# Kernel optimization log

Measured on AMD Instinct MI355X. Metric: run time of the kernel, lower is better.

The kernel has to match this reference:

```python
import jax, jax.numpy as jnp
import numpy as np

DIM = 256
K = 16
EPS = 1e-5
B, N = 8, 2048


def setup_inputs() -> dict:
    key = jax.random.key(0)
    ks = jax.random.split(key, 24)
    D = DIM
    w = lambda i, shape: jax.random.normal(ks[i], shape, dtype=jnp.float32) * 0.05
    inp = {
        "x": jax.random.normal(ks[0], (B, N, D), dtype=jnp.float32) * 0.1,
        "pos": jax.random.normal(ks[1], (B, N, 3), dtype=jnp.float32),
        # to_q / to_k / to_v (torch Linear, no bias): weight (out, in)
        "Wq": w(2, (D, D)),
        "Wk": w(3, (D, D)),
        "Wv": w(4, (D, D)),
        # pos_mlp: Conv2d(3->D,1x1,no bias), BN(D), ReLU, Conv2d(D->D,1x1,no bias)
        "pm_w1": w(5, (D, 3)),
        "pm_g1": jnp.ones((D,), jnp.float32),
        "pm_b1": w(6, (D,)),
        "pm_m1": w(7, (D,)),
        "pm_v1": jax.random.uniform(ks[8], (D,), jnp.float32) + 0.5,
        "pm_w2": w(9, (D, D)),
        # attn_mlp: Conv2d(D->D), BN(D), ReLU, Conv2d(D->D)
        "am_w1": w(10, (D, D)),
        "am_g1": jnp.ones((D,), jnp.float32),
        "am_b1": w(11, (D,)),
        "am_m1": w(12, (D,)),
        "am_v1": jax.random.uniform(ks[13], (D,), jnp.float32) + 0.5,
        "am_w2": w(14, (D, D)),
        # final_linear (with bias)
        "Wf": w(15, (D, D)),
        "bf": w(16, (D,)),
    }
    return inp


def _bn(h, g, b, m, v):
    # eval-mode BatchNorm over channel (last) dim
    return (h - m) * jax.lax.rsqrt(v + EPS) * g + b


def reference(x, pos, Wq, Wk, Wv, pm_w1, pm_g1, pm_b1, pm_m1, pm_v1, pm_w2,
              am_w1, am_g1, am_b1, am_m1, am_v1, am_w2, Wf, bf):
    D = x.shape[-1]
    # kNN over squared euclidean distance (self included, as in kNN_torch)
    sq = jnp.sum(pos * pos, axis=-1)                       # (B,N)
    dist = sq[:, :, None] + sq[:, None, :] - 2.0 * jnp.einsum('bnc,bmc->bnm', pos, pos)
    knn_idx = jax.lax.top_k(-dist, K)[1]                   # (B,N,K)

    gather = jax.vmap(lambda f, i: f[i])                   # batched index_points
    knn_xyz = gather(pos, knn_idx)                         # (B,N,K,3)

    q = jnp.einsum('bnd,ed->bne', x, Wq)                   # (B,N,D)
    k = gather(jnp.einsum('bnd,ed->bne', x, Wk), knn_idx)  # (B,N,K,D)
    v = gather(jnp.einsum('bnd,ed->bne', x, Wv), knn_idx)  # (B,N,K,D)

    rel = pos[:, :, None] - knn_xyz                        # (B,N,K,3)
    pe = jnp.einsum('bnkc,dc->bnkd', rel, pm_w1)
    pe = jax.nn.relu(_bn(pe, pm_g1, pm_b1, pm_m1, pm_v1))
    pe = jnp.einsum('bnkc,dc->bnkd', pe, pm_w2)            # (B,N,K,D)

    a = q[:, :, None] - k + pe                             # (B,N,K,D)
    a = jnp.einsum('bnkc,dc->bnkd', a, am_w1)
    a = jax.nn.relu(_bn(a, am_g1, am_b1, am_m1, am_v1))
    a = jnp.einsum('bnkc,dc->bnkd', a, am_w2)

    attn = jax.nn.softmax(a / np.sqrt(D).astype(np.float32), axis=-2)  # softmax over K
    agg = jnp.sum(attn * (v + pe), axis=2)                 # (B,N,D)
    return jnp.einsum('bnd,ed->bne', agg, Wf) + bf + x
```

## Files before the change

### kernel.cpp

```cpp
#include <hip/hip_runtime.h>
#include <math.h>

#define DIM   256
#define KNN   16
#define NPTS  2048
#define NB    8
#define TOTPTS (NB * NPTS)
#define RSB   528

typedef __attribute__((ext_vector_type(8))) short bf16x8;
typedef __attribute__((ext_vector_type(4))) float f32x4;

__device__ __forceinline__ unsigned short f2b(float f) {
    unsigned u = __builtin_bit_cast(unsigned, f);
    return (unsigned short)((u + 0x7fffu + ((u >> 16) & 1u)) >> 16);
}
__device__ __forceinline__ unsigned pack2(float a, float b) {
    return (unsigned)f2b(a) | ((unsigned)f2b(b) << 16);
}

#define OFF_KNN 0u
#define OFF_Q   (1u << 20)
#define OFF_K   ((1u << 20) + (16u << 20))
#define OFF_V   ((1u << 20) + (32u << 20))
#define OFF_WB  (49u << 20)
#define OFF_PAR (OFF_WB + 7u * 65536u * 2u)

__global__ void prep_kernel(const float* __restrict__ Wq, const float* __restrict__ Wk,
                            const float* __restrict__ Wv, const float* __restrict__ pm_w2,
                            const float* __restrict__ am_w1, const float* __restrict__ am_w2,
                            const float* __restrict__ Wf,
                            const float* __restrict__ pm_g1, const float* __restrict__ pm_b1,
                            const float* __restrict__ pm_m1, const float* __restrict__ pm_v1,
                            const float* __restrict__ am_g1, const float* __restrict__ am_b1,
                            const float* __restrict__ am_m1, const float* __restrict__ am_v1,
                            unsigned short* __restrict__ wb,
                            float* __restrict__ pm_sc, float* __restrict__ pm_bo,
                            float* __restrict__ am_sc, float* __restrict__ am_bo) {
    const int tid = blockIdx.x * 256 + threadIdx.x;
    const float* srcs[7] = {Wq, Wk, Wv, pm_w2, am_w1, am_w2, Wf};
    for (int i = tid; i < 7 * 65536; i += gridDim.x * 256) {
        const int m = i >> 16, o = i & 65535;
        wb[i] = f2b(srcs[m][o]);
    }
    if (tid < 256) {
        float s = pm_g1[tid] * rsqrtf(pm_v1[tid] + 1e-5f);
        pm_sc[tid] = s;
        pm_bo[tid] = pm_b1[tid] - pm_m1[tid] * s;
        s = am_g1[tid] * rsqrtf(am_v1[tid] + 1e-5f);
        am_sc[tid] = s;
        am_bo[tid] = am_b1[tid] - am_m1[tid] * s;
    }
}

__global__ __launch_bounds__(256, 4)
void knn_kernel(const float* __restrict__ pos, int* __restrict__ knn_out) {
    const int pt = blockIdx.x;
    const int b  = pt >> 11;
    const int n  = pt & (NPTS - 1);
    const int t  = threadIdx.x;
    const float* __restrict__ posb = pos + (size_t)b * NPTS * 3;

    const float qx = posb[n * 3 + 0], qy = posb[n * 3 + 1], qz = posb[n * 3 + 2];
    const float sqn = __fadd_rn(__fadd_rn(__fmul_rn(qx, qx), __fmul_rn(qy, qy)),
                                __fmul_rn(qz, qz));
    float d[8];
    #pragma unroll
    for (int i = 0; i < 8; ++i) {
        const int m = t + (i << 8);
        const float mx = posb[m * 3 + 0], my = posb[m * 3 + 1], mz = posb[m * 3 + 2];
        const float sqm = __fadd_rn(__fadd_rn(__fmul_rn(mx, mx), __fmul_rn(my, my)),
                                    __fmul_rn(mz, mz));
        const float dot = __fadd_rn(__fadd_rn(__fmul_rn(qx, mx), __fmul_rn(qy, my)),
                                    __fmul_rn(qz, mz));
        d[i] = __fsub_rn(__fadd_rn(sqn, sqm), __fmul_rn(2.0f, dot));
    }

    __shared__ float sd[4];
    __shared__ int   sm[4];
    __shared__ int   swin;
    unsigned mask = 0;

    for (int r = 0; r < KNN; ++r) {
        float bd = 1e30f;
        int   bm = 0x7fffffff;
        #pragma unroll
        for (int i = 0; i < 8; ++i) {
            if (!((mask >> i) & 1u)) {
                const int m = t + (i << 8);
                if (d[i] < bd || (d[i] == bd && m < bm)) { bd = d[i]; bm = m; }
            }
        }
        #pragma unroll
        for (int off = 32; off >= 1; off >>= 1) {
            const float od = __shfl_xor(bd, off);
            const int   om = __shfl_xor(bm, off);
            if (od < bd || (od == bd && om < bm)) { bd = od; bm = om; }
        }
        const int w = t >> 6;
        if ((t & 63) == 0) { sd[w] = bd; sm[w] = bm; }
        __syncthreads();
        if (t == 0) {
            float fd = sd[0]; int fm = sm[0];
            #pragma unroll
            for (int w2 = 1; w2 < 4; ++w2)
                if (sd[w2] < fd || (sd[w2] == fd && sm[w2] < fm)) { fd = sd[w2]; fm = sm[w2]; }
            swin = fm;
            knn_out[(size_t)pt * KNN + r] = fm;
        }
        __syncthreads();
        const int win = swin;
        if ((win & 255) == t) mask |= 1u << (win >> 8);
        __syncthreads();
    }
}

__device__ __forceinline__ void mfma_stage(const unsigned char* __restrict__ act,
                                           const unsigned short* __restrict__ Wb,
                                           int qr, int sub, int cbase,
                                           f32x4 acc[4][4]) {
    #pragma unroll
    for (int kk = 0; kk < 8; ++kk) {
        const int kb = kk * 64 + sub * 16;
        bf16x8 afr[4], bfr[4];
        #pragma unroll
        for (int rt = 0; rt < 4; ++rt)
            afr[rt] = *(const bf16x8*)(act + (rt * 16 + qr) * RSB + kb);
        #pragma unroll
        for (int ct = 0; ct < 4; ++ct)
            bfr[ct] = *(const bf16x8*)(Wb + (size_t)(cbase + ct * 16 + qr) * DIM + kk * 32 + sub * 8);
        #pragma unroll
        for (int rt = 0; rt < 4; ++rt)
            #pragma unroll
            for (int ct = 0; ct < 4; ++ct)
                acc[rt][ct] = __builtin_amdgcn_mfma_f32_16x16x32_bf16(afr[rt], bfr[ct],
                                                                      acc[rt][ct], 0, 0, 0);
    }
}

__global__ __launch_bounds__(256, 2)
void qkv_mfma(const float* __restrict__ X, const unsigned short* __restrict__ wb,
              float* __restrict__ Q, float* __restrict__ Kf, float* __restrict__ Vf) {
    __shared__ uint4 act4[64 * RSB / 16];
    unsigned char* act = (unsigned char*)act4;
    const int t = threadIdx.x, lane = t & 63, w = t >> 6;
    const int qr = lane & 15, sub = lane >> 4;
    const int m0 = blockIdx.x * 64;
    const int mat = blockIdx.y;
    const unsigned short* __restrict__ Wb = wb + (size_t)mat * 65536;
    float* __restrict__ O = (mat == 0) ? Q : (mat == 1) ? Kf : Vf;

    {
        const int r = t >> 2;
        const float* __restrict__ src = X + (size_t)(m0 + r) * DIM;
        #pragma unroll
        for (int j = 0; j < 8; ++j) {
            const int col = (t & 3) * 8 + j * 32;
            const float4 f0 = *(const float4*)(src + col);
            const float4 f1 = *(const float4*)(src + col + 4);
            uint4 u;
            u.x = pack2(f0.x, f0.y); u.y = pack2(f0.z, f0.w);
            u.z = pack2(f1.x, f1.y); u.w = pack2(f1.z, f1.w);
            *(uint4*)(act + r * RSB + col * 2) = u;
        }
    }
    __syncthreads();

    f32x4 acc[4][4];
    #pragma unroll
    for (int rt = 0; rt < 4; ++rt)
        #pragma unroll
        for (int ct = 0; ct < 4; ++ct) acc[rt][ct] = (f32x4)(0.0f);

    mfma_stage(act, Wb, qr, sub, w * 64, acc);

    #pragma unroll
    for (int rt = 0; rt < 4; ++rt)
        #pragma unroll
        for (int ct = 0; ct < 4; ++ct) {
            const int c = w * 64 + ct * 16 + qr;
            #pragma unroll
            for (int reg = 0; reg < 4; ++reg)
                O[(size_t)(m0 + rt * 16 + sub * 4 + reg) * DIM + c] = acc[rt][ct][reg];
        }
}

__global__ __launch_bounds__(256, 2)
void fused_attn(const float* __restrict__ x, const float* __restrict__ pos,
                const int* __restrict__ knn,
                const float* __restrict__ qf, const float* __restrict__ kf,
                const float* __restrict__ vf,
                const unsigned short* __restrict__ wb,
                const float* __restrict__ pm_w1,
                const float* __restrict__ pm_sc, const float* __restrict__ pm_bo,
                const float* __restrict__ am_sc, const float* __restrict__ am_bo,
                const float* __restrict__ bfin,
                float* __restrict__ out) {
    __shared__ uint4 act4[64 * RSB / 16];
    __shared__ int   nb_lds[64];
    __shared__ float4 rel_lds[64];
    unsigned char* act = (unsigned char*)act4;

    const int t = threadIdx.x, lane = t & 63, w = t >> 6;
    const int qr = lane & 15, sub = lane >> 4;
    const int pt_base = blockIdx.x << 2;
    const int bbase = pt_base & ~(NPTS - 1);
    const int cbase = w * 64;

    if (t < 64) {
        const int pi = t >> 4;
        const int j = knn[(size_t)(pt_base + pi) * KNN + (t & 15)];
        nb_lds[t] = j;
        const float* __restrict__ pp = pos + (size_t)(pt_base + pi) * 3;
        const float* __restrict__ pj = pos + (size_t)(bbase + j) * 3;
        rel_lds[t] = make_float4(pp[0] - pj[0], pp[1] - pj[1], pp[2] - pj[2], 0.0f);
    }
    __syncthreads();

    {
        const int c = t;
        const float w0 = pm_w1[c * 3 + 0], w1 = pm_w1[c * 3 + 1], w2 = pm_w1[c * 3 + 2];
        const float sc = pm_sc[c], bo = pm_bo[c];
        for (int r = 0; r < 64; ++r) {
            const float4 rl = rel_lds[r];
            float h = fmaf(rl.z, w2, fmaf(rl.y, w1, rl.x * w0));
            h = fmaxf(fmaf(h, sc, bo), 0.0f);
            *(unsigned short*)(act + r * RSB + c * 2) = f2b(h);
        }
    }
    __syncthreads();

    f32x4 peacc[4][4];
    #pragma unroll
    for (int rt = 0; rt < 4; ++rt)
        #pragma unroll
        for (int ct = 0; ct < 4; ++ct) peacc[rt][ct] = (f32x4)(0.0f);
    mfma_stage(act, wb + 3u * 65536u, qr, sub, cbase, peacc);
    __syncthreads();

    int nbr[4][4];
    #pragma unroll
    for (int rt = 0; rt < 4; ++rt)
        #pragma unroll
        for (int reg = 0; reg < 4; ++reg)
            nbr[rt][reg] = nb_lds[rt * 16 + sub * 4 + reg];

    #pragma unroll
    for (int rt = 0; rt < 4; ++rt)
        #pragma unroll
        for (int ct = 0; ct < 4; ++ct) {
            const int c = cbase + ct * 16 + qr;
            const float qv = qf[(size_t)(pt_base + rt) * DIM + c];
            #pragma unroll
            for (int reg = 0; reg < 4; ++reg) {
                const float kv = kf[(size_t)(bbase + nbr[rt][reg]) * DIM + c];
                const float a0 = qv - kv + peacc[rt][ct][reg];
                *(unsigned short*)(act + (rt * 16 + sub * 4 + reg) * RSB + c * 2) = f2b(a0);
            }
        }
    __syncthreads();

    f32x4 acc2[4][4];
    #pragma unroll
    for (int rt = 0; rt < 4; ++rt)
        #pragma unroll
        for (int ct = 0; ct < 4; ++ct) acc2[rt][ct] = (f32x4)(0.0f);
    mfma_stage(act, wb + 4u * 65536u, qr, sub, cbase, acc2);
    __syncthreads();
    #pragma unroll
    for (int ct = 0; ct < 4; ++ct) {
        const int c = cbase + ct * 16 + qr;
        const float sc = am_sc[c], bo = am_bo[c];
        #pragma unroll
        for (int rt = 0; rt < 4; ++rt)
            #pragma unroll
            for (int reg = 0; reg < 4; ++reg) {
                const float h = fmaxf(fmaf(acc2[rt][ct][reg], sc, bo), 0.0f);
                *(unsigned short*)(act + (rt * 16 + sub * 4 + reg) * RSB + c * 2) = f2b(h);
            }
    }
    __syncthreads();

    #pragma unroll
    for (int rt = 0; rt < 4; ++rt)
        #pragma unroll
        for (int ct = 0; ct < 4; ++ct) acc2[rt][ct] = (f32x4)(0.0f);
    mfma_stage(act, wb + 5u * 65536u, qr, sub, cbase, acc2);

    #pragma unroll
    for (int rt = 0; rt < 4; ++rt)
        #pragma unroll
        for (int ct = 0; ct < 4; ++ct) {
            float m = -1e30f;
            #pragma unroll
            for (int reg = 0; reg < 4; ++reg) {
                acc2[rt][ct][reg] *= 0.0625f;
                m = fmaxf(m, acc2[rt][ct][reg]);
            }
            m = fmaxf(m, __shfl_xor(m, 16));
            m = fmaxf(m, __shfl_xor(m, 32));
            float s = 0.0f;
            #pragma unroll
            for (int reg = 0; reg < 4; ++reg) {
                const float e = __expf(acc2[rt][ct][reg] - m);
                acc2[rt][ct][reg] = e;
                s += e;
            }
            s += __shfl_xor(s, 16);
            s += __shfl_xor(s, 32);
            const float inv = 1.0f / s;
            #pragma unroll
            for (int reg = 0; reg < 4; ++reg) acc2[rt][ct][reg] *= inv;
        }

    float agg[4][4];
    #pragma unroll
    for (int rt = 0; rt < 4; ++rt)
        #pragma unroll
        for (int ct = 0; ct < 4; ++ct) {
            const int c = cbase + ct * 16 + qr;
            float p = 0.0f;
            #pragma unroll
            for (int reg = 0; reg < 4; ++reg) {
                const float vv = vf[(size_t)(bbase + nbr[rt][reg]) * DIM + c];
                p = fmaf(acc2[rt][ct][reg], vv + peacc[rt][ct][reg], p);
            }
            p += __shfl_xor(p, 16);
            p += __shfl_xor(p, 32);
            agg[rt][ct] = p;
        }
    __syncthreads();

    {
        unsigned* actw = (unsigned*)act;
        for (int i = t; i < 12 * RSB / 4; i += 256) actw[RSB + i] = 0;
        if (sub == 0) {
            #pragma unroll
            for (int rt = 0; rt < 4; ++rt)
                #pragma unroll
                for (int ct = 0; ct < 4; ++ct) {
                    const int c = cbase + ct * 16 + qr;
                    *(unsigned short*)(act + rt * RSB + c * 2) = f2b(agg[rt][ct]);
                }
        }
    }
    __syncthreads();

    f32x4 facc[4];
    #pragma unroll
    for (int ct = 0; ct < 4; ++ct) facc[ct] = (f32x4)(0.0f);
    const unsigned short* __restrict__ Wfb = wb + 6u * 65536u;
    #pragma unroll
    for (int kk = 0; kk < 8; ++kk) {
        const int kb = kk * 64 + sub * 16;
        const bf16x8 af = *(const bf16x8*)(act + qr * RSB + kb);
        #pragma unroll
        for (int ct = 0; ct < 4; ++ct) {
            const bf16x8 bfr = *(const bf16x8*)(Wfb + (size_t)(cbase + ct * 16 + qr) * DIM + kk * 32 + sub * 8);
            facc[ct] = __builtin_amdgcn_mfma_f32_16x16x32_bf16(af, bfr, facc[ct], 0, 0, 0);
        }
    }
    if (sub == 0) {
        #pragma unroll
        for (int ct = 0; ct < 4; ++ct) {
            const int c = cbase + ct * 16 + qr;
            #pragma unroll
            for (int reg = 0; reg < 4; ++reg) {
                const size_t row = (size_t)(pt_base + reg) * DIM + c;
                out[row] = facc[ct][reg] + bfin[c] + x[row];
            }
        }
    }
}

extern "C" void kernel_launch(void* const* d_in, const int* in_sizes, int n_in,
                              void* d_out, int out_size, void* d_ws, size_t ws_size,
                              hipStream_t stream) {
    const float* x     = (const float*)d_in[0];
    const float* pos   = (const float*)d_in[1];
    const float* Wq    = (const float*)d_in[2];
    const float* Wk    = (const float*)d_in[3];
    const float* Wv    = (const float*)d_in[4];
    const float* pm_w1 = (const float*)d_in[5];
    const float* pm_g1 = (const float*)d_in[6];
    const float* pm_b1 = (const float*)d_in[7];
    const float* pm_m1 = (const float*)d_in[8];
    const float* pm_v1 = (const float*)d_in[9];
    const float* pm_w2 = (const float*)d_in[10];
    const float* am_w1 = (const float*)d_in[11];
    const float* am_g1 = (const float*)d_in[12];
    const float* am_b1 = (const float*)d_in[13];
    const float* am_m1 = (const float*)d_in[14];
    const float* am_v1 = (const float*)d_in[15];
    const float* am_w2 = (const float*)d_in[16];
    const float* Wf    = (const float*)d_in[17];
    const float* bfin  = (const float*)d_in[18];
    float* out = (float*)d_out;

    char* ws = (char*)d_ws;
    int*            knn_idx = (int*)(ws + OFF_KNN);
    float*          qf = (float*)(ws + OFF_Q);
    float*          kf = (float*)(ws + OFF_K);
    float*          vf = (float*)(ws + OFF_V);
    unsigned short* wb = (unsigned short*)(ws + OFF_WB);
    float*          pm_sc = (float*)(ws + OFF_PAR);
    float*          pm_bo = pm_sc + 256;
    float*          am_sc = pm_sc + 512;
    float*          am_bo = pm_sc + 768;

    prep_kernel<<<448, 256, 0, stream>>>(Wq, Wk, Wv, pm_w2, am_w1, am_w2, Wf,
                                         pm_g1, pm_b1, pm_m1, pm_v1,
                                         am_g1, am_b1, am_m1, am_v1,
                                         wb, pm_sc, pm_bo, am_sc, am_bo);
    knn_kernel<<<TOTPTS, 256, 0, stream>>>(pos, knn_idx);
    qkv_mfma<<<dim3(TOTPTS / 64, 3), 256, 0, stream>>>(x, wb, qf, kf, vf);
    fused_attn<<<TOTPTS / 4, 256, 0, stream>>>(x, pos, knn_idx, qf, kf, vf, wb,
                                               pm_w1, pm_sc, pm_bo, am_sc, am_bo,
                                               bfin, out);
}
```

Measured before the change: 685.5 us.

## Use one wavefront per query in kNN and split fused attention over 8 waves

The kNN kernel now assigns one 64-lane wavefront per query point, so each lane holds 32 distances. The top-16 selection becomes wave-local shuffle reductions in which only the lane that owned the winner rescans its values, which removes the three block barriers per round and the shared-memory reduction. The fused attention kernel moves to 512 threads, with each wave covering 32 output columns instead of 64, which halves per-wave accumulator registers and adds waves to hide latency. The cost is more registers per kNN lane (32 distances) and more waves competing for barriers in the attention block.

```diff
diff --git a/kernel.cpp b/kernel.cpp
--- a/kernel.cpp
+++ b/kernel.cpp
@@ -53,21 +53,21 @@
     }
 }
 
-__global__ __launch_bounds__(256, 4)
+__global__ __launch_bounds__(256, 8)
 void knn_kernel(const float* __restrict__ pos, int* __restrict__ knn_out) {
-    const int pt = blockIdx.x;
-    const int b  = pt >> 11;
-    const int n  = pt & (NPTS - 1);
-    const int t  = threadIdx.x;
+    const int wid  = (blockIdx.x << 2) | (threadIdx.x >> 6);
+    const int lane = threadIdx.x & 63;
+    const int b = wid >> 11;
+    const int n = wid & (NPTS - 1);
     const float* __restrict__ posb = pos + (size_t)b * NPTS * 3;
 
     const float qx = posb[n * 3 + 0], qy = posb[n * 3 + 1], qz = posb[n * 3 + 2];
     const float sqn = __fadd_rn(__fadd_rn(__fmul_rn(qx, qx), __fmul_rn(qy, qy)),
                                 __fmul_rn(qz, qz));
-    float d[8];
-    #pragma unroll
-    for (int i = 0; i < 8; ++i) {
-        const int m = t + (i << 8);
+    float d[32];
+    #pragma unroll
+    for (int i = 0; i < 32; ++i) {
+        const int m = lane + (i << 6);
         const float mx = posb[m * 3 + 0], my = posb[m * 3 + 1], mz = posb[m * 3 + 2];
         const float sqm = __fadd_rn(__fadd_rn(__fmul_rn(mx, mx), __fmul_rn(my, my)),
                                     __fmul_rn(mz, mz));
@@ -76,42 +76,60 @@
         d[i] = __fsub_rn(__fadd_rn(sqn, sqm), __fmul_rn(2.0f, dot));
     }
 
-    __shared__ float sd[4];
-    __shared__ int   sm[4];
-    __shared__ int   swin;
-    unsigned mask = 0;
-
+    unsigned claimed = 0;
+    float bd = d[0];
+    int   bm = lane;
+    #pragma unroll
+    for (int i = 1; i < 32; ++i) {
+        const int m = lane + (i << 6);
+        if (d[i] < bd || (d[i] == bd && m < bm)) { bd = d[i]; bm = m; }
+    }
+
+    int keep = 0;
     for (int r = 0; r < KNN; ++r) {
-        float bd = 1e30f;
-        int   bm = 0x7fffffff;
-        #pragma unroll
-        for (int i = 0; i < 8; ++i) {
-            if (!((mask >> i) & 1u)) {
-                const int m = t + (i << 8);
-                if (d[i] < bd || (d[i] == bd && m < bm)) { bd = d[i]; bm = m; }
-            }
-        }
+        float wd = bd;
+        int   wm = bm;
         #pragma unroll
         for (int off = 32; off >= 1; off >>= 1) {
-            const float od = __shfl_xor(bd, off);
-            const int   om = __shfl_xor(bm, off);
-            if (od < bd || (od == bd && om < bm)) { bd = od; bm = om; }
-        }
-        const int w = t >> 6;
-        if ((t & 63) == 0) { sd[w] = bd; sm[w] = bm; }
-        __syncthreads();
-        if (t == 0) {
-            float fd = sd[0]; int fm = sm[0];
-            #pragma unroll
-            for (int w2 = 1; w2 < 4; ++w2)
-                if (sd[w2] < fd || (sd[w2] == fd && sm[w2] < fm)) { fd = sd[w2]; fm = sm[w2]; }
-            swin = fm;
-            knn_out[(size_t)pt * KNN + r] = fm;
-        }
-        __syncthreads();
-        const int win = swin;
-        if ((win & 255) == t) mask |= 1u << (win >> 8);
-        __syncthreads();
+            const float od = __shfl_xor(wd, off);
+            const int   om = __shfl_xor(wm, off);
+            if (od < wd || (od == wd && om < wm)) { wd = od; wm = om; }
+        }
+        if (lane == r) keep = wm;
+        if ((wm & 63) == lane) {
+            claimed |= 1u << (wm >> 6);
+            bd = 1e30f; bm = 0x7fffffff;
+            #pragma unroll
+            for (int i = 0; i < 32; ++i) {
+                if (!((claimed >> i) & 1u)) {
+                    const int m = lane + (i << 6);
+                    if (d[i] < bd || (d[i] == bd && m < bm)) { bd = d[i]; bm = m; }
+                }
+            }
+        }
+    }
+    if (lane < KNN) knn_out[(size_t)wid * KNN + lane] = keep;
+}
+
+__device__ __forceinline__ void mfma_stage2(const unsigned char* __restrict__ act,
+                                            const unsigned short* __restrict__ Wb,
+                                            int qr, int sub, int cbase,
+                                            f32x4 acc[4][2]) {
+    #pragma unroll
+    for (int kk = 0; kk < 8; ++kk) {
+        const int kb = kk * 64 + sub * 16;
+        bf16x8 afr[4];
+        #pragma unroll
+        for (int rt = 0; rt < 4; ++rt)
+            afr[rt] = *(const bf16x8*)(act + (rt * 16 + qr) * RSB + kb);
+        #pragma unroll
+        for (int ct = 0; ct < 2; ++ct) {
+            const bf16x8 bfr = *(const bf16x8*)(Wb + (size_t)(cbase + ct * 16 + qr) * DIM + kk * 32 + sub * 8);
+            #pragma unroll
+            for (int rt = 0; rt < 4; ++rt)
+                acc[rt][ct] = __builtin_amdgcn_mfma_f32_16x16x32_bf16(afr[rt], bfr,
+                                                                      acc[rt][ct], 0, 0, 0);
+        }
     }
 }
 
@@ -185,7 +203,7 @@
         }
 }
 
-__global__ __launch_bounds__(256, 2)
+__global__ __launch_bounds__(512, 4)
 void fused_attn(const float* __restrict__ x, const float* __restrict__ pos,
                 const int* __restrict__ knn,
                 const float* __restrict__ qf, const float* __restrict__ kf,
@@ -205,7 +223,7 @@
     const int qr = lane & 15, sub = lane >> 4;
     const int pt_base = blockIdx.x << 2;
     const int bbase = pt_base & ~(NPTS - 1);
-    const int cbase = w * 64;
+    const int cbase = w * 32;
 
     if (t < 64) {
         const int pi = t >> 4;
@@ -218,10 +236,13 @@
     __syncthreads();
 
     {
-        const int c = t;
+        const int c  = t & 255;
+        const int rh = t >> 8;
         const float w0 = pm_w1[c * 3 + 0], w1 = pm_w1[c * 3 + 1], w2 = pm_w1[c * 3 + 2];
         const float sc = pm_sc[c], bo = pm_bo[c];
-        for (int r = 0; r < 64; ++r) {
+        #pragma unroll
+        for (int rr = 0; rr < 32; ++rr) {
+            const int r = rh * 32 + rr;
             const float4 rl = rel_lds[r];
             float h = fmaf(rl.z, w2, fmaf(rl.y, w1, rl.x * w0));
             h = fmaxf(fmaf(h, sc, bo), 0.0f);
@@ -230,12 +251,12 @@
     }
     __syncthreads();
 
-    f32x4 peacc[4][4];
-    #pragma unroll
-    for (int rt = 0; rt < 4; ++rt)
-        #pragma unroll
-        for (int ct = 0; ct < 4; ++ct) peacc[rt][ct] = (f32x4)(0.0f);
-    mfma_stage(act, wb + 3u * 65536u, qr, sub, cbase, peacc);
+    f32x4 peacc[4][2];
+    #pragma unroll
+    for (int rt = 0; rt < 4; ++rt)
+        #pragma unroll
+        for (int ct = 0; ct < 2; ++ct) peacc[rt][ct] = (f32x4)(0.0f);
+    mfma_stage2(act, wb + 3u * 65536u, qr, sub, cbase, peacc);
     __syncthreads();
 
     int nbr[4][4];
@@ -248,7 +269,7 @@
     #pragma unroll
     for (int rt = 0; rt < 4; ++rt)
         #pragma unroll
-        for (int ct = 0; ct < 4; ++ct) {
+        for (int ct = 0; ct < 2; ++ct) {
             const int c = cbase + ct * 16 + qr;
             const float qv = qf[(size_t)(pt_base + rt) * DIM + c];
             #pragma unroll
@@ -260,15 +281,15 @@
         }
     __syncthreads();
 
-    f32x4 acc2[4][4];
-    #pragma unroll
-    for (int rt = 0; rt < 4; ++rt)
-        #pragma unroll
-        for (int ct = 0; ct < 4; ++ct) acc2[rt][ct] = (f32x4)(0.0f);
-    mfma_stage(act, wb + 4u * 65536u, qr, sub, cbase, acc2);
-    __syncthreads();
-    #pragma unroll
-    for (int ct = 0; ct < 4; ++ct) {
+    f32x4 acc2[4][2];
+    #pragma unroll
+    for (int rt = 0; rt < 4; ++rt)
+        #pragma unroll
+        for (int ct = 0; ct < 2; ++ct) acc2[rt][ct] = (f32x4)(0.0f);
+    mfma_stage2(act, wb + 4u * 65536u, qr, sub, cbase, acc2);
+    __syncthreads();
+    #pragma unroll
+    for (int ct = 0; ct < 2; ++ct) {
         const int c = cbase + ct * 16 + qr;
         const float sc = am_sc[c], bo = am_bo[c];
         #pragma unroll
@@ -284,13 +305,13 @@
     #pragma unroll
     for (int rt = 0; rt < 4; ++rt)
         #pragma unroll
-        for (int ct = 0; ct < 4; ++ct) acc2[rt][ct] = (f32x4)(0.0f);
-    mfma_stage(act, wb + 5u * 65536u, qr, sub, cbase, acc2);
-
-    #pragma unroll
-    for (int rt = 0; rt < 4; ++rt)
-        #pragma unroll
-        for (int ct = 0; ct < 4; ++ct) {
+        for (int ct = 0; ct < 2; ++ct) acc2[rt][ct] = (f32x4)(0.0f);
+    mfma_stage2(act, wb + 5u * 65536u, qr, sub, cbase, acc2);
+
+    #pragma unroll
+    for (int rt = 0; rt < 4; ++rt)
+        #pragma unroll
+        for (int ct = 0; ct < 2; ++ct) {
             float m = -1e30f;
             #pragma unroll
             for (int reg = 0; reg < 4; ++reg) {
@@ -313,11 +334,11 @@
             for (int reg = 0; reg < 4; ++reg) acc2[rt][ct][reg] *= inv;
         }
 
-    float agg[4][4];
-    #pragma unroll
-    for (int rt = 0; rt < 4; ++rt)
-        #pragma unroll
-        for (int ct = 0; ct < 4; ++ct) {
+    float agg[4][2];
+    #pragma unroll
+    for (int rt = 0; rt < 4; ++rt)
+        #pragma unroll
+        for (int ct = 0; ct < 2; ++ct) {
             const int c = cbase + ct * 16 + qr;
             float p = 0.0f;
             #pragma unroll
@@ -333,12 +354,12 @@
 
     {
         unsigned* actw = (unsigned*)act;
-        for (int i = t; i < 12 * RSB / 4; i += 256) actw[RSB + i] = 0;
+        for (int i = t; i < 12 * (RSB / 4); i += 512) actw[4 * (RSB / 4) + i] = 0;
         if (sub == 0) {
             #pragma unroll
             for (int rt = 0; rt < 4; ++rt)
                 #pragma unroll
-                for (int ct = 0; ct < 4; ++ct) {
+                for (int ct = 0; ct < 2; ++ct) {
                     const int c = cbase + ct * 16 + qr;
                     *(unsigned short*)(act + rt * RSB + c * 2) = f2b(agg[rt][ct]);
                 }
@@ -346,23 +367,23 @@
     }
     __syncthreads();
 
-    f32x4 facc[4];
-    #pragma unroll
-    for (int ct = 0; ct < 4; ++ct) facc[ct] = (f32x4)(0.0f);
+    f32x4 facc[2];
+    facc[0] = (f32x4)(0.0f);
+    facc[1] = (f32x4)(0.0f);
     const unsigned short* __restrict__ Wfb = wb + 6u * 65536u;
     #pragma unroll
     for (int kk = 0; kk < 8; ++kk) {
         const int kb = kk * 64 + sub * 16;
         const bf16x8 af = *(const bf16x8*)(act + qr * RSB + kb);
         #pragma unroll
-        for (int ct = 0; ct < 4; ++ct) {
+        for (int ct = 0; ct < 2; ++ct) {
             const bf16x8 bfr = *(const bf16x8*)(Wfb + (size_t)(cbase + ct * 16 + qr) * DIM + kk * 32 + sub * 8);
             facc[ct] = __builtin_amdgcn_mfma_f32_16x16x32_bf16(af, bfr, facc[ct], 0, 0, 0);
         }
     }
     if (sub == 0) {
         #pragma unroll
-        for (int ct = 0; ct < 4; ++ct) {
+        for (int ct = 0; ct < 2; ++ct) {
             const int c = cbase + ct * 16 + qr;
             #pragma unroll
             for (int reg = 0; reg < 4; ++reg) {
@@ -412,9 +433,9 @@
                                          pm_g1, pm_b1, pm_m1, pm_v1,
                                          am_g1, am_b1, am_m1, am_v1,
                                          wb, pm_sc, pm_bo, am_sc, am_bo);
-    knn_kernel<<<TOTPTS, 256, 0, stream>>>(pos, knn_idx);
+    knn_kernel<<<TOTPTS / 4, 256, 0, stream>>>(pos, knn_idx);
     qkv_mfma<<<dim3(TOTPTS / 64, 3), 256, 0, stream>>>(x, wb, qf, kf, vf);
-    fused_attn<<<TOTPTS / 4, 256, 0, stream>>>(x, pos, knn_idx, qf, kf, vf, wb,
+    fused_attn<<<TOTPTS / 4, 512, 0, stream>>>(x, pos, knn_idx, qf, kf, vf, wb,
                                                pm_w1, pm_sc, pm_bo, am_sc, am_bo,
                                                bfin, out);
 }
```

Result: slower. 1.175 ms (+71.4%).
